# Optimization experiments

Hardware: AMD Instinct MI355X
Metric: run time of the kernel (lower is better)

Reference implementation:

```python
import jax, jax.numpy as jnp
import numpy as np

N, M, APP, ANOISE = 65536, 16, 48, 0.01


def _norm(x):
    return x / (jnp.linalg.norm(x, axis=-1, keepdims=True) + 1e-8)


def setup_inputs() -> dict:
    ks = jax.random.split(jax.random.key(0), 16)
    xyzs = jax.random.normal(ks[0], (N, 3), jnp.float32)
    app_features = 0.1 * jax.random.normal(ks[1], (N, APP), jnp.float32)
    viewdirs = _norm(jax.random.normal(ks[2], (N, 3), jnp.float32))
    normals = _norm(jax.random.normal(ks[3], (N, 3), jnp.float32))
    feat_noise = jax.random.normal(ks[4], (N, APP), jnp.float32)
    u = jax.random.uniform(ks[5], (N, M, 2), jnp.float32, 1e-4, 1.0 - 1e-4)
    bounce_mask = jax.random.uniform(ks[6], (N,)) < 0.4
    ray_mask = (jax.random.uniform(ks[7], (N, M)) < 0.5) & bounce_mask[:, None]
    DIN, BIN, HID = 3 + 3 + APP, 5 * 3 + APP + 1, 128
    Wd1 = jax.random.normal(ks[8], (DIN, HID), jnp.float32) / np.sqrt(DIN)
    bd1 = jnp.zeros((HID,), jnp.float32)
    Wd2 = jax.random.normal(ks[9], (HID, 9), jnp.float32) / np.sqrt(HID)
    bd2 = jnp.zeros((9,), jnp.float32)
    Wb1 = jax.random.normal(ks[10], (BIN, HID), jnp.float32) / np.sqrt(BIN)
    bb1 = jnp.zeros((HID,), jnp.float32)
    Wb2 = jax.random.normal(ks[11], (HID, 3), jnp.float32) / np.sqrt(HID)
    bb2 = jnp.zeros((3,), jnp.float32)
    return dict(xyzs=xyzs, app_features=app_features, viewdirs=viewdirs,
                normals=normals, feat_noise=feat_noise, u=u,
                Wd1=Wd1, bd1=bd1, Wd2=Wd2, bd2=bd2,
                Wb1=Wb1, bb1=bb1, Wb2=Wb2, bb2=bb2,
                bounce_mask=bounce_mask, ray_mask=ray_mask)


def reference(xyzs, app_features, viewdirs, normals, feat_noise, u,
              Wd1, bd1, Wd2, bd2, Wb1, bb1, Wb2, bb2,
              bounce_mask, ray_mask):
    sg = jax.lax.stop_gradient
    noise_feats = app_features + feat_noise * ANOISE  # [N, APP]

    # diffuse module: MLP(xyz, viewdir, features) -> diffuse, tint, matprop
    din = jnp.concatenate([xyzs, viewdirs, app_features], axis=-1)
    h = jax.nn.relu(din @ Wd1 + bd1)
    dout = h @ Wd2 + bd2  # [N, 9]
    diffuse = jax.nn.sigmoid(dout[:, 0:3])
    r1 = jax.nn.sigmoid(dout[:, 6]) * 0.98 + 0.01  # roughness in (0.01, 0.99)

    bV = -viewdirs
    bN = _norm(normals)

    # per-point orthonormal world basis (columns: tangent, bitangent, normal)
    up = jnp.where(jnp.abs(bN[:, 2:3]) < 0.99,
                   jnp.asarray([0.0, 0.0, 1.0], bN.dtype),
                   jnp.asarray([1.0, 0.0, 0.0], bN.dtype))
    t = _norm(jnp.cross(up, bN))
    b = jnp.cross(bN, t)
    basis = jnp.stack([t, b, bN], axis=-1)  # [N, 3, 3], basis @ local = world

    # GGX half-vector sampling with a = r1^2
    a2 = (r1 ** 2)[:, None] ** 2  # [N, 1]
    u1, u2 = u[..., 0], u[..., 1]  # [N, M]
    cos_t = jnp.sqrt((1.0 - u1) / (1.0 + (a2 - 1.0) * u1))
    sin_t = jnp.sqrt(jnp.clip(1.0 - cos_t * cos_t, 0.0, None))
    phi = 2.0 * jnp.pi * u2
    Hl = jnp.stack([sin_t * jnp.cos(phi), sin_t * jnp.sin(phi), cos_t], axis=-1)
    H = jnp.einsum('nij,nmj->nmi', basis, Hl)  # world-space half vectors [N, M, 3]
    Vm = bV[:, None, :]
    L = _norm(2.0 * jnp.sum(Vm * H, axis=-1, keepdims=True) * H - Vm)  # [N, M, 3]

    # local-frame vectors (basis^T v)
    halfvec = jnp.einsum('nji,nmj->nmi', basis, H)
    diffvec = jnp.einsum('nji,nmj->nmi', basis, L)

    # mip level from (detached) roughness; env-map style incoming light
    mipval = sg(jnp.log(jnp.clip(a2, 1e-6, None)))  # [N, 1]
    sky = jnp.asarray([1.0, 0.9, 0.8], L.dtype)
    incoming = (jnp.maximum(L[..., 2:3], 0.0) * sky + 0.1) \
        * jnp.exp(0.1 * mipval)[..., None]  # [N, M, 3]

    # BRDF MLP over all (point, ray) pairs; mask applied in the reduction
    eV = jnp.broadcast_to(Vm, L.shape)
    eN = jnp.broadcast_to(bN[:, None, :], L.shape)
    ea1 = jnp.broadcast_to(r1[:, None, None], (L.shape[0], L.shape[1], 1))
    efeat = jnp.broadcast_to(noise_feats[:, None, :],
                             (L.shape[0], L.shape[1], noise_feats.shape[-1]))
    bin_ = jnp.concatenate([eV, sg(L), sg(eN), sg(halfvec), sg(diffvec),
                            efeat, sg(ea1)], axis=-1)  # [N, M, 64]
    hb = jax.nn.relu(bin_ @ Wb1 + bb1)
    brdf_weight = jax.nn.sigmoid(hb @ Wb2 + bb2)  # [N, M, 3]

    # row_mask_sum / ray_count, scattered back to bounce points
    maskf = ray_mask.astype(brdf_weight.dtype)[..., None]  # [N, M, 1]
    ray_count = maskf.sum(axis=1) + 1e-8  # [N, 1]
    tinted_ref_rgb = (incoming * brdf_weight * maskf).sum(axis=1) / ray_count
    reflect_rgb = jnp.where(bounce_mask[:, None], tinted_ref_rgb, 0.0)
    rgb = reflect_rgb + diffuse
    return rgb
```

## Files before the change

kernel.cpp:

```cpp
#include <hip/hip_runtime.h>
#include <hip/hip_bf16.h>
#include <math.h>

#define MRAY 16
#define BLOCK 256
#define GRID 4096

typedef float f2 __attribute__((ext_vector_type(2)));
typedef float f4 __attribute__((ext_vector_type(4)));
typedef _Float16 h8 __attribute__((ext_vector_type(8)));
typedef _Float16 h4 __attribute__((ext_vector_type(4)));
typedef __fp16 fp16x2 __attribute__((ext_vector_type(2)));

__device__ __forceinline__ float sigmoidf_(float x){ return 1.0f/(1.0f+__expf(-x)); }
__device__ __forceinline__ f2 shflxor2(f2 v, int off){
    f2 r; r.x = __shfl_xor(v.x, off); r.y = __shfl_xor(v.y, off); return r;
}
__device__ __forceinline__ f4 mfma16(h8 a, h8 b, f4 c){
    return __builtin_amdgcn_mfma_f32_16x16x32_f16(a, b, c, 0, 0, 0);
}
__device__ __forceinline__ f4 mfma16k16(h4 a, h4 b, f4 c){
    return __builtin_amdgcn_mfma_f32_16x16x16f16(a, b, c, 0, 0, 0);
}
__device__ __forceinline__ int pkh(float a, float b){
    union { fp16x2 h; int i; } u;
    u.h = __builtin_amdgcn_cvt_pkrtz(a, b);
    return u.i;
}

__global__ __launch_bounds__(256) void prep(
    const float* __restrict__ Wd1, const float* __restrict__ Wb1,
    const float* __restrict__ Wb2, const float* __restrict__ Wd2,
    const unsigned int* __restrict__ rm, float* __restrict__ ws)
{
    const int gt = blockIdx.x*256 + threadIdx.x;
    h8* fragDT  = (h8*)(ws + 16);
    h8* fragB   = fragDT + 1024;
    h8* fragRT  = fragB + 1024;
    h4* fragW2  = (h4*)(ws + 10256);
    h4* fragWd2t= (h4*)(ws + 11280);
    if (gt < 1024){
        int ks = gt >> 9, t = (gt >> 6) & 7, l = gt & 63;
        int j = 16*t + (l & 15), gg = (l >> 4) & 3;
        h8 v;
        #pragma unroll
        for (int b = 0; b < 8; b++){
            int k = 32*ks + 8*gg + b;
            int row = (k < 48) ? 6 + k : (k < 54 ? k - 48 : -1);
            v[b] = (_Float16)(row >= 0 ? Wd1[row*128 + j] : 0.0f);
        }
        fragDT[gt] = v;
    } else if (gt < 2048){
        int e = gt - 1024;
        int ks = e >> 9, t = (e >> 6) & 7, l = e & 63;
        int col = 16*t + (l & 15), gg = (l >> 4) & 3;
        h8 v;
        #pragma unroll
        for (int b = 0; b < 8; b++){
            int k = 32*ks + 8*gg + b;
            int row = (k < 48) ? 15 + k : (k < 51 ? k - 48 : (k < 54 ? k - 45 : -1));
            v[b] = (_Float16)(row >= 0 ? Wb1[row*128 + col] : 0.0f);
        }
        fragB[e] = v;
    } else if (gt < 2560){
        int e = gt - 2048;
        int t = e >> 6, l = e & 63;
        int j = 16*t + (l & 15), gg = (l >> 4) & 3;
        h8 v;
        #pragma unroll
        for (int b = 0; b < 8; b++){
            int k = 8*gg + b;
            int row = (k < 3) ? 3 + k : (k < 9 ? 6 + k : (k == 9 ? 63 : -1));
            v[b] = (_Float16)(row >= 0 ? Wb1[row*128 + j] : 0.0f);
        }
        fragRT[e] = v;
    } else if (gt < 3072){
        int e = gt - 2560;
        int t = e >> 6, l = e & 63;
        int r = l & 15, kg = (l >> 4) & 3;
        int c = r & 3;
        h4 v;
        #pragma unroll
        for (int i = 0; i < 4; i++){
            int j = 16*t + 4*kg + i;
            v[i] = (_Float16)((c < 3) ? Wb2[j*3 + c] : 0.0f);
        }
        fragW2[e] = v;
    } else if (gt < 3584){
        int e = gt - 3072;
        int t = e >> 6, l = e & 63;
        int r = l & 15, kg = (l >> 4) & 3;
        int c = r & 3;
        int col = (c == 3) ? 6 : c;
        h4 v;
        #pragma unroll
        for (int i = 0; i < 4; i++){
            int j = 16*t + 4*kg + i;
            v[i] = (_Float16)Wd2[j*9 + col];
        }
        fragWd2t[e] = v;
    } else if (gt >= 3584 && gt < 3648){
        int l = gt - 3584;
        bool bad=false, isf32=false, odd_nz=false, even_one=false;
        #pragma unroll
        for (int i = 0; i < 8; i++){
            int idx = l*8 + i;
            unsigned v = rm[idx];
            if (v != 0u && v != 1u && v != 0x3F800000u) bad = true;
            if (v == 0x3F800000u) isf32 = true;
            if ((idx & 1) && v != 0u) odd_nz = true;
            if (!(idx & 1) && v != 0u) even_one = true;
        }
        unsigned long long Bb = __ballot(bad);
        unsigned long long Bf = __ballot(isf32);
        unsigned long long Bo = __ballot(odd_nz);
        unsigned long long Be = __ballot(even_one);
        if (l == 0){
            int f;
            if (Bb) f = 0;
            else if (Bf) f = 1;
            else if (!Bo && Be) f = 2;
            else f = 1;
            ((int*)ws)[0] = f;
        }
    }
}

__global__ __launch_bounds__(BLOCK, 2) void rb_main(
    const float* __restrict__ xyzs, const float* __restrict__ app,
    const float* __restrict__ vdirs, const float* __restrict__ normals,
    const float* __restrict__ noise, const float* __restrict__ uu,
    const float* __restrict__ bd1, const float* __restrict__ bd2,
    const float* __restrict__ bb1, const float* __restrict__ bb2,
    const void* __restrict__ raym, const float* __restrict__ wsf,
    float* __restrict__ out)
{
    __shared__ float baseL[16*132];
    __shared__ float psum[4][16][4];

    const int tid  = threadIdx.x;
    const int lane = tid & 63;
    const int ch   = __builtin_amdgcn_readfirstlane(tid >> 6);
    const int pbase = blockIdx.x * 16;

    const int flag = ((const int*)wsf)[0];
    const h8* fragDT  = (const h8*)(wsf + 16);
    const h8* fragB   = fragDT + 1024;
    const h8* fragRT  = fragB + 1024;
    const h4* fragW2  = (const h4*)(wsf + 10256);
    const h4* fragWd2t= (const h4*)(wsf + 11280);

    const int c15 = lane & 15;
    const int kg  = lane >> 4;
    const int myp = 4*ch + kg;
    const int myn = pbase + myp;

    f2 uv = *(const f2*)&uu[(myn*MRAY + c15)*2];
    float mf0;
    {
        int midx = myn*MRAY + c15;
        bool mk;
        if (flag == 0)      mk = ((const unsigned char*)raym)[midx] != 0;
        else if (flag == 2) mk = ((const unsigned long long*)raym)[midx] != 0ull;
        else                mk = ((const unsigned int*)raym)[midx] != 0u;
        mf0 = mk ? 1.f : 0.f;
    }

    float bas[9], Vlx, Vly, Vlz;
    {
        float nx = normals[myn*3+0], ny = normals[myn*3+1], nz = normals[myn*3+2];
        float inv = 1.0f/(sqrtf(nx*nx+ny*ny+nz*nz)+1e-8f);
        float bx = nx*inv, by = ny*inv, bz = nz*inv;
        float ux, uy, uz;
        if (fabsf(bz) < 0.99f){ ux=0.f; uy=0.f; uz=1.f; } else { ux=1.f; uy=0.f; uz=0.f; }
        float tx = uy*bz-uz*by, ty = uz*bx-ux*bz, tz = ux*by-uy*bx;
        float tin = 1.0f/(sqrtf(tx*tx+ty*ty+tz*tz)+1e-8f);
        tx*=tin; ty*=tin; tz*=tin;
        float ex = by*tz-bz*ty, ey = bz*tx-bx*tz, ez = bx*ty-by*tx;
        bas[0]=tx; bas[1]=ex; bas[2]=bx;
        bas[3]=ty; bas[4]=ey; bas[5]=by;
        bas[6]=tz; bas[7]=ez; bas[8]=bz;
        float vx = vdirs[myn*3+0], vy = vdirs[myn*3+1], vz = vdirs[myn*3+2];
        Vlx = -(tx*vx + ty*vy + tz*vz);
        Vly = -(ex*vx + ey*vy + ez*vz);
        Vlz = -(bx*vx + by*vy + bz*vz);
    }

    const int n_p = pbase + c15;
    float xv0=0.f,xv1=0.f,xv2=0.f,vv0=0.f,vv1=0.f,vv2=0.f;
    if (kg == 2){
        xv0 = xyzs[n_p*3+0]; xv1 = xyzs[n_p*3+1]; xv2 = xyzs[n_p*3+2];
        vv0 = vdirs[n_p*3+0]; vv1 = vdirs[n_p*3+1]; vv2 = vdirs[n_p*3+2];
    }
    float bn0, bn1, bn2;
    {
        float nx = normals[n_p*3+0], ny = normals[n_p*3+1], nz = normals[n_p*3+2];
        float inv = 1.0f/(sqrtf(nx*nx+ny*ny+nz*nz)+1e-8f);
        bn0 = nx*inv; bn1 = ny*inv; bn2 = nz*inv;
    }
    const float* ap = app + n_p*48;
    const float* nz = noise + n_p*48;
    h8 afD[2], afB[2];
    #pragma unroll
    for (int ks = 0; ks < 2; ks++){
        const int k0 = 32*ks + 8*kg;
        union { int i[4]; h8 h; } UD, UB;
        if (k0 <= 40){
            f4 a0 = *(const f4*)(ap + k0);
            f4 a1 = *(const f4*)(ap + k0 + 4);
            f4 z0 = *(const f4*)(nz + k0);
            f4 z1 = *(const f4*)(nz + k0 + 4);
            UD.i[0] = pkh(a0.x, a0.y); UD.i[1] = pkh(a0.z, a0.w);
            UD.i[2] = pkh(a1.x, a1.y); UD.i[3] = pkh(a1.z, a1.w);
            UB.i[0] = pkh(fmaf(0.01f,z0.x,a0.x), fmaf(0.01f,z0.y,a0.y));
            UB.i[1] = pkh(fmaf(0.01f,z0.z,a0.z), fmaf(0.01f,z0.w,a0.w));
            UB.i[2] = pkh(fmaf(0.01f,z1.x,a1.x), fmaf(0.01f,z1.y,a1.y));
            UB.i[3] = pkh(fmaf(0.01f,z1.z,a1.z), fmaf(0.01f,z1.w,a1.w));
        } else if (k0 == 48){
            UD.i[0] = pkh(xv0, xv1); UD.i[1] = pkh(xv2, vv0);
            UD.i[2] = pkh(vv1, vv2); UD.i[3] = 0;
            UB.i[0] = pkh(-vv0, -vv1); UB.i[1] = pkh(-vv2, bn0);
            UB.i[2] = pkh(bn1, bn2);   UB.i[3] = 0;
        } else {
            UD.i[0]=0; UD.i[1]=0; UD.i[2]=0; UD.i[3]=0;
            UB.i[0]=0; UB.i[1]=0; UB.i[2]=0; UB.i[3]=0;
        }
        afD[ks]=UD.h; afB[ks]=UB.h;
    }

    f4 S1 = {0.f,0.f,0.f,0.f};
    #pragma unroll
    for (int tt = 0; tt < 2; tt++){
        const int t = 2*ch + tt;
        const int j0 = 16*t + 4*kg;
        f4 C = *(const f4*)&bd1[j0];
        f4 d = mfma16(fragDT[t*64 + lane], afD[0], C);
        d = mfma16(fragDT[512 + t*64 + lane], afD[1], d);
        f4 z = {0.f,0.f,0.f,0.f};
        d = __builtin_elementwise_max(d, z);
        union { int i[2]; h4 h; } B2;
        B2.i[0] = pkh(d.x, d.y);
        B2.i[1] = pkh(d.z, d.w);
        S1 = mfma16k16(fragWd2t[t*64 + lane], B2.h, S1);
    }
    if (kg == 0)
        *(f4*)&psum[ch][c15][0] = S1;

    #pragma unroll
    for (int tt = 0; tt < 2; tt++){
        const int t = 2*ch + tt;
        const int col = 16*t + c15;
        float bias = bb1[col];
        f4 D = {bias,bias,bias,bias};
        D = mfma16(afB[0], fragB[t*64 + lane], D);
        D = mfma16(afB[1], fragB[512 + t*64 + lane], D);
        baseL[(4*kg+0)*132 + col] = D.x;
        baseL[(4*kg+1)*132 + col] = D.y;
        baseL[(4*kg+2)*132 + col] = D.z;
        baseL[(4*kg+3)*132 + col] = D.w;
    }

    __syncthreads();

    f4 sv = *(const f4*)&psum[0][myp][0];
    sv += *(const f4*)&psum[1][myp][0];
    sv += *(const f4*)&psum[2][myp][0];
    sv += *(const f4*)&psum[3][myp][0];
    const float dd0 = sigmoidf_(sv.x + bd2[0]);
    const float dd1 = sigmoidf_(sv.y + bd2[1]);
    const float dd2 = sigmoidf_(sv.z + bd2[2]);
    const float r1o = sigmoidf_(sv.w + bd2[6])*0.98f + 0.01f;
    float a2s = r1o*r1o; a2s = a2s*a2s;
    const float sclo = __expf(0.1f*__logf(fmaxf(a2s, 1e-6f)));

    float ct = sqrtf((1.0f-uv.x)/(1.0f+(a2s-1.0f)*uv.x));
    float st = sqrtf(fmaxf(1.0f-ct*ct,0.0f));
    float phi = 6.28318530717958647692f*uv.y;
    float hl0 = st*__cosf(phi), hl1 = st*__sinf(phi), hl2 = ct;
    float dvh = Vlx*hl0 + Vly*hl1 + Vlz*hl2;
    float t2 = dvh + dvh;
    float llx = fmaf(t2,hl0,-Vlx), lly = fmaf(t2,hl1,-Vly), llz = fmaf(t2,hl2,-Vlz);
    float linv = 1.0f/(sqrtf(llx*llx+lly*lly+llz*llz)+1e-8f);
    llx*=linv; lly*=linv; llz*=linv;
    float rv2w = bas[6]*llx + bas[7]*lly + bas[8]*llz;
    int w0 = pkh(bas[0]*llx + bas[1]*lly + bas[2]*llz,
                 bas[3]*llx + bas[4]*lly + bas[5]*llz);
    int w1 = pkh(rv2w, hl0);
    int w2 = pkh(hl1, hl2);
    int w3 = pkh(llx, lly);
    int w4 = pkh(llz, r1o);

    h8 af[4];
    #pragma unroll
    for (int pp = 0; pp < 4; pp++){
        const int srcl = pp*16 + c15;
        int u0 = __shfl(w0, srcl), u1 = __shfl(w1, srcl);
        int u2 = __shfl(w2, srcl), u3 = __shfl(w3, srcl);
        int u4 = __shfl(w4, srcl);
        const bool g0 = (kg == 0), g1 = (kg == 1);
        union { int i[4]; h8 h; } U;
        U.i[0] = g0 ? u0 : (g1 ? u4 : 0);
        U.i[1] = g0 ? u1 : 0;
        U.i[2] = g0 ? u2 : 0;
        U.i[3] = g0 ? u3 : 0;
        af[pp] = U.h;
    }

    f4 S2[4];
    #pragma unroll
    for (int pp = 0; pp < 4; pp++) S2[pp] = f4{0.f,0.f,0.f,0.f};

    #pragma unroll 4
    for (int t = 0; t < 8; t++){
        const int j0 = 16*t + 4*kg;
        h8 Af = fragRT[t*64 + lane];
        h4 Wf = fragW2[t*64 + lane];
        #pragma unroll
        for (int pp = 0; pp < 4; pp++){
            f4 C = *(const f4*)&baseL[(4*ch+pp)*132 + j0];
            f4 d = mfma16(Af, af[pp], C);
            f4 z = {0.f,0.f,0.f,0.f};
            d = __builtin_elementwise_max(d, z);
            union { int i[2]; h4 h; } B2;
            B2.i[0] = pkh(d.x, d.y);
            B2.i[1] = pkh(d.z, d.w);
            S2[pp] = mfma16k16(Wf, B2.h, S2[pp]);
        }
    }

    f4 slo = (kg & 1) ? S2[1] : S2[0];
    f4 shi = (kg & 1) ? S2[3] : S2[2];
    f4 sS  = (kg & 2) ? shi : slo;

    float e0 = sigmoidf_(sS.x + bb2[0]);
    float e1 = sigmoidf_(sS.y + bb2[1]);
    float e2 = sigmoidf_(sS.z + bb2[2]);
    float lzp = fmaxf(rv2w, 0.f);
    f2 pA = { (lzp*1.0f+0.1f)*sclo*e0*mf0, (lzp*0.9f+0.1f)*sclo*e1*mf0 };
    f2 pB = { (lzp*0.8f+0.1f)*sclo*e2*mf0, mf0 };
    #pragma unroll
    for (int off = 1; off <= 8; off <<= 1){
        pA += shflxor2(pA, off);
        pB += shflxor2(pB, off);
    }
    if (c15 == 0){
        float den = pB.y + 1e-8f;
        out[myn*3+0] = pA.x/den + dd0;
        out[myn*3+1] = pA.y/den + dd1;
        out[myn*3+2] = pB.x/den + dd2;
    }
}

extern "C" void kernel_launch(void* const* d_in, const int* in_sizes, int n_in,
                              void* d_out, int out_size, void* d_ws, size_t ws_size,
                              hipStream_t stream) {
    const float* xyzs    = (const float*)d_in[0];
    const float* app     = (const float*)d_in[1];
    const float* vdirs   = (const float*)d_in[2];
    const float* normals = (const float*)d_in[3];
    const float* noise   = (const float*)d_in[4];
    const float* uu      = (const float*)d_in[5];
    const float* Wd1     = (const float*)d_in[6];
    const float* bd1     = (const float*)d_in[7];
    const float* Wd2     = (const float*)d_in[8];
    const float* bd2     = (const float*)d_in[9];
    const float* Wb1     = (const float*)d_in[10];
    const float* bb1     = (const float*)d_in[11];
    const float* Wb2     = (const float*)d_in[12];
    const float* bb2     = (const float*)d_in[13];
    const void*  raym    = d_in[15];
    float* wsf = (float*)d_ws;
    float* out = (float*)d_out;

    prep<<<16, 256, 0, stream>>>(Wd1, Wb1, Wb2, Wd2, (const unsigned int*)raym, wsf);
    rb_main<<<GRID, BLOCK, 0, stream>>>(xyzs, app, vdirs, normals, noise, uu,
                                        bd1, bd2, bb1, bb2,
                                        raym, wsf, out);
}
```

Baseline: 47.38 us.

## Process four point groups per block and apply ReLU in packed fp16

The grid shrinks from 4096 to 1024 blocks, and each block now loops over four 16-point groups, with a trailing barrier so shared memory can be reused safely between iterations. The ReLU after each MFMA moves from an fp32 vector max to a packed fp16 max applied after the pkrtz conversion. The loop spreads block launch overhead over more work. It also adds an extra __syncthreads per group and serialises work that used to be spread across more blocks, which can reduce latency hiding.

```diff
diff --git a/kernel.cpp b/kernel.cpp
--- a/kernel.cpp
+++ b/kernel.cpp
@@ -4,7 +4,8 @@
 
 #define MRAY 16
 #define BLOCK 256
-#define GRID 4096
+#define GRID 1024
+#define GPB 4
 
 typedef float f2 __attribute__((ext_vector_type(2)));
 typedef float f4 __attribute__((ext_vector_type(4)));
@@ -25,6 +26,12 @@
 __device__ __forceinline__ int pkh(float a, float b){
     union { fp16x2 h; int i; } u;
     u.h = __builtin_amdgcn_cvt_pkrtz(a, b);
+    return u.i;
+}
+__device__ __forceinline__ int relu2h(int w){
+    union { int i; fp16x2 h; } u; u.i = w;
+    fp16x2 z = {(__fp16)0.f, (__fp16)0.f};
+    u.h = __builtin_elementwise_max(u.h, z);
     return u.i;
 }
 
@@ -141,7 +148,6 @@
     const int tid  = threadIdx.x;
     const int lane = tid & 63;
     const int ch   = __builtin_amdgcn_readfirstlane(tid >> 6);
-    const int pbase = blockIdx.x * 16;
 
     const int flag = ((const int*)wsf)[0];
     const h8* fragDT  = (const h8*)(wsf + 16);
@@ -152,202 +158,204 @@
 
     const int c15 = lane & 15;
     const int kg  = lane >> 4;
-    const int myp = 4*ch + kg;
-    const int myn = pbase + myp;
-
-    f2 uv = *(const f2*)&uu[(myn*MRAY + c15)*2];
-    float mf0;
-    {
-        int midx = myn*MRAY + c15;
-        bool mk;
-        if (flag == 0)      mk = ((const unsigned char*)raym)[midx] != 0;
-        else if (flag == 2) mk = ((const unsigned long long*)raym)[midx] != 0ull;
-        else                mk = ((const unsigned int*)raym)[midx] != 0u;
-        mf0 = mk ? 1.f : 0.f;
-    }
-
-    float bas[9], Vlx, Vly, Vlz;
-    {
-        float nx = normals[myn*3+0], ny = normals[myn*3+1], nz = normals[myn*3+2];
-        float inv = 1.0f/(sqrtf(nx*nx+ny*ny+nz*nz)+1e-8f);
-        float bx = nx*inv, by = ny*inv, bz = nz*inv;
-        float ux, uy, uz;
-        if (fabsf(bz) < 0.99f){ ux=0.f; uy=0.f; uz=1.f; } else { ux=1.f; uy=0.f; uz=0.f; }
-        float tx = uy*bz-uz*by, ty = uz*bx-ux*bz, tz = ux*by-uy*bx;
-        float tin = 1.0f/(sqrtf(tx*tx+ty*ty+tz*tz)+1e-8f);
-        tx*=tin; ty*=tin; tz*=tin;
-        float ex = by*tz-bz*ty, ey = bz*tx-bx*tz, ez = bx*ty-by*tx;
-        bas[0]=tx; bas[1]=ex; bas[2]=bx;
-        bas[3]=ty; bas[4]=ey; bas[5]=by;
-        bas[6]=tz; bas[7]=ez; bas[8]=bz;
-        float vx = vdirs[myn*3+0], vy = vdirs[myn*3+1], vz = vdirs[myn*3+2];
-        Vlx = -(tx*vx + ty*vy + tz*vz);
-        Vly = -(ex*vx + ey*vy + ez*vz);
-        Vlz = -(bx*vx + by*vy + bz*vz);
-    }
-
-    const int n_p = pbase + c15;
-    float xv0=0.f,xv1=0.f,xv2=0.f,vv0=0.f,vv1=0.f,vv2=0.f;
-    if (kg == 2){
-        xv0 = xyzs[n_p*3+0]; xv1 = xyzs[n_p*3+1]; xv2 = xyzs[n_p*3+2];
-        vv0 = vdirs[n_p*3+0]; vv1 = vdirs[n_p*3+1]; vv2 = vdirs[n_p*3+2];
-    }
-    float bn0, bn1, bn2;
-    {
-        float nx = normals[n_p*3+0], ny = normals[n_p*3+1], nz = normals[n_p*3+2];
-        float inv = 1.0f/(sqrtf(nx*nx+ny*ny+nz*nz)+1e-8f);
-        bn0 = nx*inv; bn1 = ny*inv; bn2 = nz*inv;
-    }
-    const float* ap = app + n_p*48;
-    const float* nz = noise + n_p*48;
-    h8 afD[2], afB[2];
-    #pragma unroll
-    for (int ks = 0; ks < 2; ks++){
-        const int k0 = 32*ks + 8*kg;
-        union { int i[4]; h8 h; } UD, UB;
-        if (k0 <= 40){
-            f4 a0 = *(const f4*)(ap + k0);
-            f4 a1 = *(const f4*)(ap + k0 + 4);
-            f4 z0 = *(const f4*)(nz + k0);
-            f4 z1 = *(const f4*)(nz + k0 + 4);
-            UD.i[0] = pkh(a0.x, a0.y); UD.i[1] = pkh(a0.z, a0.w);
-            UD.i[2] = pkh(a1.x, a1.y); UD.i[3] = pkh(a1.z, a1.w);
-            UB.i[0] = pkh(fmaf(0.01f,z0.x,a0.x), fmaf(0.01f,z0.y,a0.y));
-            UB.i[1] = pkh(fmaf(0.01f,z0.z,a0.z), fmaf(0.01f,z0.w,a0.w));
-            UB.i[2] = pkh(fmaf(0.01f,z1.x,a1.x), fmaf(0.01f,z1.y,a1.y));
-            UB.i[3] = pkh(fmaf(0.01f,z1.z,a1.z), fmaf(0.01f,z1.w,a1.w));
-        } else if (k0 == 48){
-            UD.i[0] = pkh(xv0, xv1); UD.i[1] = pkh(xv2, vv0);
-            UD.i[2] = pkh(vv1, vv2); UD.i[3] = 0;
-            UB.i[0] = pkh(-vv0, -vv1); UB.i[1] = pkh(-vv2, bn0);
-            UB.i[2] = pkh(bn1, bn2);   UB.i[3] = 0;
-        } else {
-            UD.i[0]=0; UD.i[1]=0; UD.i[2]=0; UD.i[3]=0;
-            UB.i[0]=0; UB.i[1]=0; UB.i[2]=0; UB.i[3]=0;
-        }
-        afD[ks]=UD.h; afB[ks]=UB.h;
-    }
-
-    f4 S1 = {0.f,0.f,0.f,0.f};
-    #pragma unroll
-    for (int tt = 0; tt < 2; tt++){
-        const int t = 2*ch + tt;
-        const int j0 = 16*t + 4*kg;
-        f4 C = *(const f4*)&bd1[j0];
-        f4 d = mfma16(fragDT[t*64 + lane], afD[0], C);
-        d = mfma16(fragDT[512 + t*64 + lane], afD[1], d);
-        f4 z = {0.f,0.f,0.f,0.f};
-        d = __builtin_elementwise_max(d, z);
-        union { int i[2]; h4 h; } B2;
-        B2.i[0] = pkh(d.x, d.y);
-        B2.i[1] = pkh(d.z, d.w);
-        S1 = mfma16k16(fragWd2t[t*64 + lane], B2.h, S1);
-    }
-    if (kg == 0)
-        *(f4*)&psum[ch][c15][0] = S1;
-
-    #pragma unroll
-    for (int tt = 0; tt < 2; tt++){
-        const int t = 2*ch + tt;
-        const int col = 16*t + c15;
-        float bias = bb1[col];
-        f4 D = {bias,bias,bias,bias};
-        D = mfma16(afB[0], fragB[t*64 + lane], D);
-        D = mfma16(afB[1], fragB[512 + t*64 + lane], D);
-        baseL[(4*kg+0)*132 + col] = D.x;
-        baseL[(4*kg+1)*132 + col] = D.y;
-        baseL[(4*kg+2)*132 + col] = D.z;
-        baseL[(4*kg+3)*132 + col] = D.w;
-    }
-
-    __syncthreads();
-
-    f4 sv = *(const f4*)&psum[0][myp][0];
-    sv += *(const f4*)&psum[1][myp][0];
-    sv += *(const f4*)&psum[2][myp][0];
-    sv += *(const f4*)&psum[3][myp][0];
-    const float dd0 = sigmoidf_(sv.x + bd2[0]);
-    const float dd1 = sigmoidf_(sv.y + bd2[1]);
-    const float dd2 = sigmoidf_(sv.z + bd2[2]);
-    const float r1o = sigmoidf_(sv.w + bd2[6])*0.98f + 0.01f;
-    float a2s = r1o*r1o; a2s = a2s*a2s;
-    const float sclo = __expf(0.1f*__logf(fmaxf(a2s, 1e-6f)));
-
-    float ct = sqrtf((1.0f-uv.x)/(1.0f+(a2s-1.0f)*uv.x));
-    float st = sqrtf(fmaxf(1.0f-ct*ct,0.0f));
-    float phi = 6.28318530717958647692f*uv.y;
-    float hl0 = st*__cosf(phi), hl1 = st*__sinf(phi), hl2 = ct;
-    float dvh = Vlx*hl0 + Vly*hl1 + Vlz*hl2;
-    float t2 = dvh + dvh;
-    float llx = fmaf(t2,hl0,-Vlx), lly = fmaf(t2,hl1,-Vly), llz = fmaf(t2,hl2,-Vlz);
-    float linv = 1.0f/(sqrtf(llx*llx+lly*lly+llz*llz)+1e-8f);
-    llx*=linv; lly*=linv; llz*=linv;
-    float rv2w = bas[6]*llx + bas[7]*lly + bas[8]*llz;
-    int w0 = pkh(bas[0]*llx + bas[1]*lly + bas[2]*llz,
-                 bas[3]*llx + bas[4]*lly + bas[5]*llz);
-    int w1 = pkh(rv2w, hl0);
-    int w2 = pkh(hl1, hl2);
-    int w3 = pkh(llx, lly);
-    int w4 = pkh(llz, r1o);
-
-    h8 af[4];
-    #pragma unroll
-    for (int pp = 0; pp < 4; pp++){
-        const int srcl = pp*16 + c15;
-        int u0 = __shfl(w0, srcl), u1 = __shfl(w1, srcl);
-        int u2 = __shfl(w2, srcl), u3 = __shfl(w3, srcl);
-        int u4 = __shfl(w4, srcl);
-        const bool g0 = (kg == 0), g1 = (kg == 1);
-        union { int i[4]; h8 h; } U;
-        U.i[0] = g0 ? u0 : (g1 ? u4 : 0);
-        U.i[1] = g0 ? u1 : 0;
-        U.i[2] = g0 ? u2 : 0;
-        U.i[3] = g0 ? u3 : 0;
-        af[pp] = U.h;
-    }
-
-    f4 S2[4];
-    #pragma unroll
-    for (int pp = 0; pp < 4; pp++) S2[pp] = f4{0.f,0.f,0.f,0.f};
-
-    #pragma unroll 4
-    for (int t = 0; t < 8; t++){
-        const int j0 = 16*t + 4*kg;
-        h8 Af = fragRT[t*64 + lane];
-        h4 Wf = fragW2[t*64 + lane];
+
+    for (int grp = 0; grp < GPB; grp++){
+        const int pbase = (blockIdx.x * GPB + grp) * 16;
+        const int myp = 4*ch + kg;
+        const int myn = pbase + myp;
+
+        f2 uv = *(const f2*)&uu[(myn*MRAY + c15)*2];
+        float mf0;
+        {
+            int midx = myn*MRAY + c15;
+            bool mk;
+            if (flag == 0)      mk = ((const unsigned char*)raym)[midx] != 0;
+            else if (flag == 2) mk = ((const unsigned long long*)raym)[midx] != 0ull;
+            else                mk = ((const unsigned int*)raym)[midx] != 0u;
+            mf0 = mk ? 1.f : 0.f;
+        }
+
+        float bas[9], Vlx, Vly, Vlz;
+        {
+            float nx = normals[myn*3+0], ny = normals[myn*3+1], nz2 = normals[myn*3+2];
+            float inv = 1.0f/(sqrtf(nx*nx+ny*ny+nz2*nz2)+1e-8f);
+            float bx = nx*inv, by = ny*inv, bz = nz2*inv;
+            float ux, uy, uz;
+            if (fabsf(bz) < 0.99f){ ux=0.f; uy=0.f; uz=1.f; } else { ux=1.f; uy=0.f; uz=0.f; }
+            float tx = uy*bz-uz*by, ty = uz*bx-ux*bz, tz = ux*by-uy*bx;
+            float tin = 1.0f/(sqrtf(tx*tx+ty*ty+tz*tz)+1e-8f);
+            tx*=tin; ty*=tin; tz*=tin;
+            float ex = by*tz-bz*ty, ey = bz*tx-bx*tz, ez = bx*ty-by*tx;
+            bas[0]=tx; bas[1]=ex; bas[2]=bx;
+            bas[3]=ty; bas[4]=ey; bas[5]=by;
+            bas[6]=tz; bas[7]=ez; bas[8]=bz;
+            float vx = vdirs[myn*3+0], vy = vdirs[myn*3+1], vz = vdirs[myn*3+2];
+            Vlx = -(tx*vx + ty*vy + tz*vz);
+            Vly = -(ex*vx + ey*vy + ez*vz);
+            Vlz = -(bx*vx + by*vy + bz*vz);
+        }
+
+        const int n_p = pbase + c15;
+        float xv0=0.f,xv1=0.f,xv2=0.f,vv0=0.f,vv1=0.f,vv2=0.f;
+        if (kg == 2){
+            xv0 = xyzs[n_p*3+0]; xv1 = xyzs[n_p*3+1]; xv2 = xyzs[n_p*3+2];
+            vv0 = vdirs[n_p*3+0]; vv1 = vdirs[n_p*3+1]; vv2 = vdirs[n_p*3+2];
+        }
+        float bn0, bn1, bn2;
+        {
+            float nx = normals[n_p*3+0], ny = normals[n_p*3+1], nz2 = normals[n_p*3+2];
+            float inv = 1.0f/(sqrtf(nx*nx+ny*ny+nz2*nz2)+1e-8f);
+            bn0 = nx*inv; bn1 = ny*inv; bn2 = nz2*inv;
+        }
+        const float* ap = app + n_p*48;
+        const float* nz = noise + n_p*48;
+        h8 afD[2], afB[2];
+        #pragma unroll
+        for (int ks = 0; ks < 2; ks++){
+            const int k0 = 32*ks + 8*kg;
+            union { int i[4]; h8 h; } UD, UB;
+            if (k0 <= 40){
+                f4 a0 = *(const f4*)(ap + k0);
+                f4 a1 = *(const f4*)(ap + k0 + 4);
+                f4 z0 = *(const f4*)(nz + k0);
+                f4 z1 = *(const f4*)(nz + k0 + 4);
+                UD.i[0] = pkh(a0.x, a0.y); UD.i[1] = pkh(a0.z, a0.w);
+                UD.i[2] = pkh(a1.x, a1.y); UD.i[3] = pkh(a1.z, a1.w);
+                UB.i[0] = pkh(fmaf(0.01f,z0.x,a0.x), fmaf(0.01f,z0.y,a0.y));
+                UB.i[1] = pkh(fmaf(0.01f,z0.z,a0.z), fmaf(0.01f,z0.w,a0.w));
+                UB.i[2] = pkh(fmaf(0.01f,z1.x,a1.x), fmaf(0.01f,z1.y,a1.y));
+                UB.i[3] = pkh(fmaf(0.01f,z1.z,a1.z), fmaf(0.01f,z1.w,a1.w));
+            } else if (k0 == 48){
+                UD.i[0] = pkh(xv0, xv1); UD.i[1] = pkh(xv2, vv0);
+                UD.i[2] = pkh(vv1, vv2); UD.i[3] = 0;
+                UB.i[0] = pkh(-vv0, -vv1); UB.i[1] = pkh(-vv2, bn0);
+                UB.i[2] = pkh(bn1, bn2);   UB.i[3] = 0;
+            } else {
+                UD.i[0]=0; UD.i[1]=0; UD.i[2]=0; UD.i[3]=0;
+                UB.i[0]=0; UB.i[1]=0; UB.i[2]=0; UB.i[3]=0;
+            }
+            afD[ks]=UD.h; afB[ks]=UB.h;
+        }
+
+        f4 S1 = {0.f,0.f,0.f,0.f};
+        #pragma unroll
+        for (int tt = 0; tt < 2; tt++){
+            const int t = 2*ch + tt;
+            const int j0 = 16*t + 4*kg;
+            f4 C = *(const f4*)&bd1[j0];
+            f4 d = mfma16(fragDT[t*64 + lane], afD[0], C);
+            d = mfma16(fragDT[512 + t*64 + lane], afD[1], d);
+            union { int i[2]; h4 h; } B2;
+            B2.i[0] = relu2h(pkh(d.x, d.y));
+            B2.i[1] = relu2h(pkh(d.z, d.w));
+            S1 = mfma16k16(fragWd2t[t*64 + lane], B2.h, S1);
+        }
+        if (kg == 0)
+            *(f4*)&psum[ch][c15][0] = S1;
+
+        #pragma unroll
+        for (int tt = 0; tt < 2; tt++){
+            const int t = 2*ch + tt;
+            const int col = 16*t + c15;
+            float bias = bb1[col];
+            f4 D = {bias,bias,bias,bias};
+            D = mfma16(afB[0], fragB[t*64 + lane], D);
+            D = mfma16(afB[1], fragB[512 + t*64 + lane], D);
+            baseL[(4*kg+0)*132 + col] = D.x;
+            baseL[(4*kg+1)*132 + col] = D.y;
+            baseL[(4*kg+2)*132 + col] = D.z;
+            baseL[(4*kg+3)*132 + col] = D.w;
+        }
+
+        __syncthreads();
+
+        f4 sv = *(const f4*)&psum[0][myp][0];
+        sv += *(const f4*)&psum[1][myp][0];
+        sv += *(const f4*)&psum[2][myp][0];
+        sv += *(const f4*)&psum[3][myp][0];
+        const float dd0 = sigmoidf_(sv.x + bd2[0]);
+        const float dd1 = sigmoidf_(sv.y + bd2[1]);
+        const float dd2 = sigmoidf_(sv.z + bd2[2]);
+        const float r1o = sigmoidf_(sv.w + bd2[6])*0.98f + 0.01f;
+        float a2s = r1o*r1o; a2s = a2s*a2s;
+        const float sclo = __expf(0.1f*__logf(fmaxf(a2s, 1e-6f)));
+
+        float ct = sqrtf((1.0f-uv.x)/(1.0f+(a2s-1.0f)*uv.x));
+        float st = sqrtf(fmaxf(1.0f-ct*ct,0.0f));
+        float phi = 6.28318530717958647692f*uv.y;
+        float hl0 = st*__cosf(phi), hl1 = st*__sinf(phi), hl2 = ct;
+        float dvh = Vlx*hl0 + Vly*hl1 + Vlz*hl2;
+        float t2 = dvh + dvh;
+        float llx = fmaf(t2,hl0,-Vlx), lly = fmaf(t2,hl1,-Vly), llz = fmaf(t2,hl2,-Vlz);
+        float linv = 1.0f/(sqrtf(llx*llx+lly*lly+llz*llz)+1e-8f);
+        llx*=linv; lly*=linv; llz*=linv;
+        float rv2w = bas[6]*llx + bas[7]*lly + bas[8]*llz;
+        int w0 = pkh(bas[0]*llx + bas[1]*lly + bas[2]*llz,
+                     bas[3]*llx + bas[4]*lly + bas[5]*llz);
+        int w1 = pkh(rv2w, hl0);
+        int w2 = pkh(hl1, hl2);
+        int w3 = pkh(llx, lly);
+        int w4 = pkh(llz, r1o);
+
+        h8 af[4];
         #pragma unroll
         for (int pp = 0; pp < 4; pp++){
-            f4 C = *(const f4*)&baseL[(4*ch+pp)*132 + j0];
-            f4 d = mfma16(Af, af[pp], C);
-            f4 z = {0.f,0.f,0.f,0.f};
-            d = __builtin_elementwise_max(d, z);
-            union { int i[2]; h4 h; } B2;
-            B2.i[0] = pkh(d.x, d.y);
-            B2.i[1] = pkh(d.z, d.w);
-            S2[pp] = mfma16k16(Wf, B2.h, S2[pp]);
-        }
-    }
-
-    f4 slo = (kg & 1) ? S2[1] : S2[0];
-    f4 shi = (kg & 1) ? S2[3] : S2[2];
-    f4 sS  = (kg & 2) ? shi : slo;
-
-    float e0 = sigmoidf_(sS.x + bb2[0]);
-    float e1 = sigmoidf_(sS.y + bb2[1]);
-    float e2 = sigmoidf_(sS.z + bb2[2]);
-    float lzp = fmaxf(rv2w, 0.f);
-    f2 pA = { (lzp*1.0f+0.1f)*sclo*e0*mf0, (lzp*0.9f+0.1f)*sclo*e1*mf0 };
-    f2 pB = { (lzp*0.8f+0.1f)*sclo*e2*mf0, mf0 };
-    #pragma unroll
-    for (int off = 1; off <= 8; off <<= 1){
-        pA += shflxor2(pA, off);
-        pB += shflxor2(pB, off);
-    }
-    if (c15 == 0){
-        float den = pB.y + 1e-8f;
-        out[myn*3+0] = pA.x/den + dd0;
-        out[myn*3+1] = pA.y/den + dd1;
-        out[myn*3+2] = pB.x/den + dd2;
+            const int srcl = pp*16 + c15;
+            int u0 = __shfl(w0, srcl), u1 = __shfl(w1, srcl);
+            int u2 = __shfl(w2, srcl), u3 = __shfl(w3, srcl);
+            int u4 = __shfl(w4, srcl);
+            const bool g0 = (kg == 0), g1 = (kg == 1);
+            union { int i[4]; h8 h; } U;
+            U.i[0] = g0 ? u0 : (g1 ? u4 : 0);
+            U.i[1] = g0 ? u1 : 0;
+            U.i[2] = g0 ? u2 : 0;
+            U.i[3] = g0 ? u3 : 0;
+            af[pp] = U.h;
+        }
+
+        f4 S2[4];
+        #pragma unroll
+        for (int pp = 0; pp < 4; pp++) S2[pp] = f4{0.f,0.f,0.f,0.f};
+
+        #pragma unroll 4
+        for (int t = 0; t < 8; t++){
+            const int j0 = 16*t + 4*kg;
+            h8 Af = fragRT[t*64 + lane];
+            h4 Wf = fragW2[t*64 + lane];
+            #pragma unroll
+            for (int pp = 0; pp < 4; pp++){
+                f4 C = *(const f4*)&baseL[(4*ch+pp)*132 + j0];
+                f4 d = mfma16(Af, af[pp], C);
+                union { int i[2]; h4 h; } B2;
+                B2.i[0] = relu2h(pkh(d.x, d.y));
+                B2.i[1] = relu2h(pkh(d.z, d.w));
+                S2[pp] = mfma16k16(Wf, B2.h, S2[pp]);
+            }
+        }
+
+        f4 slo = (kg & 1) ? S2[1] : S2[0];
+        f4 shi = (kg & 1) ? S2[3] : S2[2];
+        f4 sS  = (kg & 2) ? shi : slo;
+
+        float e0 = sigmoidf_(sS.x + bb2[0]);
+        float e1 = sigmoidf_(sS.y + bb2[1]);
+        float e2 = sigmoidf_(sS.z + bb2[2]);
+        float lzp = fmaxf(rv2w, 0.f);
+        f2 pA = { (lzp*1.0f+0.1f)*sclo*e0*mf0, (lzp*0.9f+0.1f)*sclo*e1*mf0 };
+        f2 pB = { (lzp*0.8f+0.1f)*sclo*e2*mf0, mf0 };
+        #pragma unroll
+        for (int off = 1; off <= 8; off <<= 1){
+            pA += shflxor2(pA, off);
+            pB += shflxor2(pB, off);
+        }
+        if (c15 == 0){
+            float den = pB.y + 1e-8f;
+            out[myn*3+0] = pA.x/den + dd0;
+            out[myn*3+1] = pA.y/den + dd1;
+            out[myn*3+2] = pB.x/den + dd2;
+        }
+
+        __syncthreads();
     }
 }
 
```

After: 56.49 us. 19.2% more time.
